# Kernel optimization log

Hardware: AMD Instinct MI355X
Metric: run time of the kernel (lower is better)

## Reference

```python
import jax, jax.numpy as jnp
import numpy as np

ROPE_BASE = 10000.0


def _rope_cos_sin(n, d, dtype):
    # standard llama-style rotary embedding over head dim d
    inv_freq = 1.0 / (ROPE_BASE ** (jnp.arange(0, d, 2, dtype=jnp.float32) / d))
    t = jnp.arange(n, dtype=jnp.float32)
    freqs = jnp.einsum('n,f->nf', t, inv_freq)          # [N, d/2]
    emb = jnp.concatenate([freqs, freqs], axis=-1)      # [N, d]
    return jnp.cos(emb).astype(dtype), jnp.sin(emb).astype(dtype)


def _rotate_half(x):
    x1, x2 = jnp.split(x, 2, axis=-1)
    return jnp.concatenate([-x2, x1], axis=-1)


def _apply_rope(x, cos, sin):
    # x: [B, H, N, D]; cos/sin: [N, D] broadcast over B, H
    return x * cos + _rotate_half(x) * sin


def setup_inputs() -> dict:
    key = jax.random.key(0)
    k1, k2, k3 = jax.random.split(key, 3)
    B, N, dim = 2, 2048, 1024
    heads, dim_head = 16, 64
    inner = heads * dim_head
    x = jax.random.normal(k1, (B, N, dim), dtype=jnp.float32)
    w_qkv = jax.random.normal(k2, (dim, 3 * inner), dtype=jnp.float32) * (dim ** -0.5)
    w_out = jax.random.normal(k3, (inner, dim), dtype=jnp.float32) * (inner ** -0.5)
    return {"x": x, "w_qkv": w_qkv, "w_out": w_out}


def reference(x, w_qkv, w_out):
    B, N, _ = x.shape
    heads, dim_head = 16, 64
    qkv = jnp.einsum('bnd,de->bne', x, w_qkv)
    q, k, v = jnp.split(qkv, 3, axis=-1)
    def to_heads(t):
        return t.reshape(B, N, heads, dim_head).transpose(0, 2, 1, 3)  # [B,H,N,D]
    q, k, v = to_heads(q), to_heads(k), to_heads(v)
    cos, sin = _rope_cos_sin(N, dim_head, x.dtype)
    q = _apply_rope(q, cos, sin)
    k = _apply_rope(k, cos, sin)
    scale = dim_head ** -0.5
    scores = jnp.einsum('bhqd,bhkd->bhqk', q, k) * scale   # [B,H,N,N], non-causal
    attn = jax.nn.softmax(scores, axis=-1)
    out = jnp.einsum('bhqk,bhkd->bhqd', attn, v)
    out = out.transpose(0, 2, 1, 3).reshape(B, N, heads * dim_head)
    return jnp.einsum('bne,ed->bnd', out, w_out)
```

## Files before the change

### kernel.cpp

```cpp
#include <hip/hip_runtime.h>

typedef __attribute__((ext_vector_type(8))) short bf16x8;
typedef __attribute__((ext_vector_type(4))) float f32x4;

#define MFMA(a, b, c) __builtin_amdgcn_mfma_f32_16x16x32_bf16(a, b, c, 0, 0, 0)

__device__ __forceinline__ unsigned short f2bf(float f) {
    unsigned u = __builtin_bit_cast(unsigned, f);
    u += 0x7fffu + ((u >> 16) & 1u);
    return (unsigned short)(u >> 16);
}

__device__ __forceinline__ void gload16(const unsigned short* g, unsigned short* l) {
    __builtin_amdgcn_global_load_lds(
        (const __attribute__((address_space(1))) void*)g,
        (__attribute__((address_space(3))) void*)l, 16, 0, 0);
}

__device__ __forceinline__ unsigned pack_bf16(float lo, float hi) {
    unsigned a = __builtin_bit_cast(unsigned, lo) + 0x8000u;
    unsigned b = __builtin_bit_cast(unsigned, hi) + 0x8000u;
    return __builtin_amdgcn_perm(b, a, 0x07060302);
}


__global__ __launch_bounds__(256) void cvt_bf16(const float* __restrict__ in,
                                                unsigned short* __restrict__ out, int n) {
    int i = (blockIdx.x * 256 + threadIdx.x) * 4;
    if (i < n) {
        float4 f = *(const float4*)(in + i);
        ushort4 u;
        u.x = f2bf(f.x); u.y = f2bf(f.y); u.z = f2bf(f.z); u.w = f2bf(f.w);
        *(ushort4*)(out + i) = u;
    }
}

__global__ __launch_bounds__(256) void transpose_cvt(const float* __restrict__ in,
                                                     unsigned short* __restrict__ out,
                                                     int R, int C) {
    __shared__ float tile[32][33];
    const int c0 = blockIdx.x * 32, r0 = blockIdx.y * 32;
    const int tr = threadIdx.x >> 3;
    const int j4 = (threadIdx.x & 7) * 4;
    float4 f = *(const float4*)(in + (size_t)(r0 + tr) * C + c0 + j4);
    tile[tr][j4 + 0] = f.x; tile[tr][j4 + 1] = f.y;
    tile[tr][j4 + 2] = f.z; tile[tr][j4 + 3] = f.w;
    __syncthreads();
    ushort4 u;
    u.x = f2bf(tile[j4 + 0][tr]); u.y = f2bf(tile[j4 + 1][tr]);
    u.z = f2bf(tile[j4 + 2][tr]); u.w = f2bf(tile[j4 + 3][tr]);
    *(ushort4*)(out + (size_t)(c0 + tr) * R + r0 + j4) = u;
}

__global__ __launch_bounds__(256) void rope_tab(float* __restrict__ cosT,
                                                float* __restrict__ sinT) {
    int i = blockIdx.x * 256 + threadIdx.x;
    int n = i >> 5, f = i & 31;
    float ang = (float)n * exp2f((float)f * -0.4152410118609203f);
    float s, c;
    sincosf(ang, &s, &c);
    cosT[i] = c; sinT[i] = s;
}


template <int EPI>
__global__ __launch_bounds__(256, 3) void gemm_bt(const unsigned short* __restrict__ A,
                                                  const unsigned short* __restrict__ Bt,
                                                  int K, int Ncols,
                                                  unsigned short* __restrict__ oq,
                                                  unsigned short* __restrict__ ok,
                                                  unsigned short* __restrict__ ovt,
                                                  float* __restrict__ of,
                                                  const float* __restrict__ cosT,
                                                  const float* __restrict__ sinT) {
    __shared__ unsigned short As[2][128 * 32];
    __shared__ unsigned short Bs[2][128 * 32];
    const int tid = threadIdx.x;
    const int w = tid >> 6, lane = tid & 63, quad = lane >> 4, cc = lane & 15;
    const int wm = w >> 1, wn = w & 1;
    const int m0 = blockIdx.y * 128, n0 = blockIdx.x * 128;

    size_t aoff[2], boff[2];
#pragma unroll
    for (int t = 0; t < 2; t++) {
        int S = w * 128 + t * 64 + lane;
        int row = S >> 2;
        int c = (S & 3) ^ ((row >> 1) & 3);
        aoff[t] = (size_t)(m0 + row) * K + c * 8;
        boff[t] = (size_t)(n0 + row) * K + c * 8;
    }

#pragma unroll
    for (int t = 0; t < 2; t++) {
        gload16(A + aoff[t], &As[0][(w * 2 + t) * 512]);
        gload16(Bt + boff[t], &Bs[0][(w * 2 + t) * 512]);
    }
    __syncthreads();

    f32x4 acc[4][4] = {};
    const int rpos = (quad ^ ((cc >> 1) & 3)) * 8;
    const int nkt = K >> 5;

    for (int kt = 0; kt < nkt; kt++) {
        const int pb = kt & 1;
        if (kt < nkt - 1) {
            const int ko = (kt + 1) * 32;
#pragma unroll
            for (int t = 0; t < 2; t++) {
                gload16(A + aoff[t] + ko, &As[pb ^ 1][(w * 2 + t) * 512]);
                gload16(Bt + boff[t] + ko, &Bs[pb ^ 1][(w * 2 + t) * 512]);
            }
        }
        bf16x8 af[4], bf[4];
#pragma unroll
        for (int i = 0; i < 4; i++)
            af[i] = *(const bf16x8*)&As[pb][(wm * 64 + i * 16 + cc) * 32 + rpos];
#pragma unroll
        for (int i = 0; i < 4; i++)
            bf[i] = *(const bf16x8*)&Bs[pb][(wn * 64 + i * 16 + cc) * 32 + rpos];
#pragma unroll
        for (int i = 0; i < 4; i++)
#pragma unroll
            for (int j = 0; j < 4; j++)
                acc[i][j] = MFMA(af[i], bf[j], acc[i][j]);
        __syncthreads();
    }

    if (EPI == 0) {
        const int e0 = n0 + wn * 64;
        const int which = e0 >> 10;
        const int h = (e0 >> 6) & 15;
        if (which < 2) {
            unsigned short* dst = (which == 0) ? oq : ok;
            const float postscale = (which == 0) ? 0.125f : 1.0f;
#pragma unroll
            for (int mf = 0; mf < 4; mf++) {
#pragma unroll
                for (int r = 0; r < 4; r++) {
                    int mg = m0 + wm * 64 + mf * 16 + quad * 4 + r;
                    int nseq = mg & 2047, b = mg >> 11;
                    float vals[4];
#pragma unroll
                    for (int nf = 0; nf < 4; nf++) vals[nf] = acc[mf][nf][r];
                    size_t rowbase = ((size_t)(b * 16 + h) * 2048 + nseq) * 64;
#pragma unroll
                    for (int nf = 0; nf < 4; nf++) {
                        int d = nf * 16 + cc;
                        int f = d & 31;
                        float cs = cosT[nseq * 32 + f];
                        float sn = sinT[nseq * 32 + f];
                        float partner = vals[nf ^ 2];
                        float outv = (vals[nf] * cs +
                                      ((nf < 2) ? -partner : partner) * sn) * postscale;
                        dst[rowbase + d] = f2bf(outv);
                    }
                }
            }
        } else {
#pragma unroll
            for (int mf = 0; mf < 4; mf++) {
                int mg0 = m0 + wm * 64 + mf * 16 + quad * 4;
                int b = mg0 >> 11, nseq = mg0 & 2047;
#pragma unroll
                for (int nf = 0; nf < 4; nf++) {
                    int d = nf * 16 + cc;
                    ushort4 pk;
                    pk.x = f2bf(acc[mf][nf][0]);
                    pk.y = f2bf(acc[mf][nf][1]);
                    pk.z = f2bf(acc[mf][nf][2]);
                    pk.w = f2bf(acc[mf][nf][3]);
                    *(ushort4*)(ovt + ((size_t)(b * 16 + h) * 64 + d) * 2048 + nseq) = pk;
                }
            }
        }
    } else {
#pragma unroll
        for (int mf = 0; mf < 4; mf++)
#pragma unroll
            for (int nf = 0; nf < 4; nf++)
#pragma unroll
                for (int r = 0; r < 4; r++) {
                    int mg = m0 + wm * 64 + mf * 16 + quad * 4 + r;
                    of[(size_t)mg * Ncols + n0 + wn * 64 + nf * 16 + cc] = acc[mf][nf][r];
                }
    }
}


__global__ __launch_bounds__(256, 2) void attn(const unsigned short* __restrict__ q,
                                               const unsigned short* __restrict__ k,
                                               const unsigned short* __restrict__ vt,
                                               unsigned short* __restrict__ o) {
    __shared__ unsigned short ks[2][64 * 64];
    __shared__ unsigned short vs[2][64 * 64];
    __shared__ unsigned short ps[128 * 72];
    __shared__ float rsb[128];
    const int tid = threadIdx.x;
    const int w = tid >> 6, lane = tid & 63, quad = lane >> 4, cc = lane & 15;
    const int bh = blockIdx.x & 31, qt = blockIdx.x >> 5;

    const unsigned short* qg = q + ((size_t)bh * 2048 + qt * 128 + w * 32) * 64;
    bf16x8 aq[2][2];
#pragma unroll
    for (int mf = 0; mf < 2; mf++)
#pragma unroll
        for (int kc = 0; kc < 2; kc++)
            aq[mf][kc] = *(const bf16x8*)(qg + (mf * 16 + cc) * 64 + kc * 32 + quad * 8);

    int koff[2], voff[2];
#pragma unroll
    for (int t = 0; t < 2; t++) {
        int S = w * 128 + t * 64 + lane;
        int row = S >> 3;
        int c = (S & 7) ^ (row & 7);
        koff[t] = row * 64 + c * 8;
        voff[t] = row * 2048 + c * 8;
    }

    const unsigned short* kg0 = k + (size_t)bh * 2048 * 64;
    const unsigned short* vg0 = vt + (size_t)bh * 64 * 2048;

#pragma unroll
    for (int t = 0; t < 2; t++) {
        gload16(kg0 + koff[t], &ks[0][(w * 2 + t) * 512]);
        gload16(vg0 + voff[t], &vs[0][(w * 2 + t) * 512]);
    }
    __syncthreads();

    f32x4 oacc[2][4] = {};
    float rs[2] = {};

    for (int kt = 0; kt < 32; kt++) {
        const int pb = kt & 1;
        if (kt < 31) {
            const unsigned short* kb = kg0 + (kt + 1) * 4096;
            const unsigned short* vb = vg0 + (kt + 1) * 64;
#pragma unroll
            for (int t = 0; t < 2; t++) {
                gload16(kb + koff[t], &ks[pb ^ 1][(w * 2 + t) * 512]);
                gload16(vb + voff[t], &vs[pb ^ 1][(w * 2 + t) * 512]);
            }
        }

        f32x4 s2[2][4] = {};
#pragma unroll
        for (int kc = 0; kc < 2; kc++) {
#pragma unroll
            for (int nf = 0; nf < 4; nf++) {
                bf16x8 bk = *(const bf16x8*)&ks[pb][(nf * 16 + cc) * 64 +
                                                    ((kc * 4 + quad) ^ (cc & 7)) * 8];
                s2[0][nf] = MFMA(bk, aq[0][kc], s2[0][nf]);
                s2[1][nf] = MFMA(bk, aq[1][kc], s2[1][nf]);
            }
        }

#pragma unroll
        for (int mf = 0; mf < 2; mf++) {
#pragma unroll
            for (int nf = 0; nf < 4; nf++) {
                float p0 = __builtin_amdgcn_exp2f(
                    __builtin_fmaf(s2[mf][nf][0], 1.44269504f, -11.54156036f));
                float p1 = __builtin_amdgcn_exp2f(
                    __builtin_fmaf(s2[mf][nf][1], 1.44269504f, -11.54156036f));
                float p2 = __builtin_amdgcn_exp2f(
                    __builtin_fmaf(s2[mf][nf][2], 1.44269504f, -11.54156036f));
                float p3 = __builtin_amdgcn_exp2f(
                    __builtin_fmaf(s2[mf][nf][3], 1.44269504f, -11.54156036f));
                rs[mf] += (p0 + p1) + (p2 + p3);
                uint2 pk;
                pk.x = pack_bf16(p0, p1);
                pk.y = pack_bf16(p2, p3);
                *(uint2*)&ps[(w * 32 + mf * 16 + cc) * 72 + nf * 16 + quad * 4] = pk;
            }
        }

#pragma unroll
        for (int kc = 0; kc < 2; kc++) {
            bf16x8 ap[2];
            ap[0] = *(const bf16x8*)&ps[(w * 32 + cc) * 72 + kc * 32 + quad * 8];
            ap[1] = *(const bf16x8*)&ps[(w * 32 + 16 + cc) * 72 + kc * 32 + quad * 8];
#pragma unroll
            for (int df = 0; df < 4; df++) {
                bf16x8 bv = *(const bf16x8*)&vs[pb][(df * 16 + cc) * 64 +
                                                    ((kc * 4 + quad) ^ (cc & 7)) * 8];
                oacc[0][df] = MFMA(ap[0], bv, oacc[0][df]);
                oacc[1][df] = MFMA(ap[1], bv, oacc[1][df]);
            }
        }

        __syncthreads();
    }

#pragma unroll
    for (int mf = 0; mf < 2; mf++) {
        rs[mf] += __shfl_xor(rs[mf], 16, 64);
        rs[mf] += __shfl_xor(rs[mf], 32, 64);
    }
    if (quad == 0) {
        rsb[w * 32 + cc] = rs[0];
        rsb[w * 32 + 16 + cc] = rs[1];
    }

#pragma unroll
    for (int mf = 0; mf < 2; mf++) {
        f32x4 rv = *(const f32x4*)&rsb[w * 32 + mf * 16 + quad * 4];
        f32x4 inv;
#pragma unroll
        for (int r = 0; r < 4; r++) inv[r] = 1.0f / rv[r];
#pragma unroll
        for (int r = 0; r < 4; r++)
#pragma unroll
            for (int df = 0; df < 4; df++)
                ps[(w * 32 + mf * 16 + quad * 4 + r) * 72 + df * 16 + cc] =
                    f2bf(oacc[mf][df][r] * inv[r]);
    }
    __syncthreads();
    {
        const int b = bh >> 4, h = bh & 15;
        int row = tid >> 1, hf = tid & 1;
        unsigned short* og =
            o + ((size_t)(b * 2048 + qt * 128 + row)) * 1024 + h * 64 + hf * 32;
#pragma unroll
        for (int j = 0; j < 4; j++)
            *(uint4*)(og + j * 8) = *(const uint4*)&ps[row * 72 + hf * 32 + j * 8];
    }
}


extern "C" void kernel_launch(void* const* d_in, const int* in_sizes, int n_in,
                              void* d_out, int out_size, void* d_ws, size_t ws_size,
                              hipStream_t stream) {
    const float* x = (const float*)d_in[0];
    const float* w_qkv = (const float*)d_in[1];
    const float* w_out = (const float*)d_in[2];
    float* out = (float*)d_out;

    unsigned short* xb    = (unsigned short*)d_ws;
    unsigned short* wqkvT = xb + 4096 * 1024;
    unsigned short* woutT = wqkvT + 3072 * 1024;
    unsigned short* qb    = woutT + 1024 * 1024;
    unsigned short* kb    = qb + 2 * 16 * 2048 * 64;
    unsigned short* vtb   = kb + 2 * 16 * 2048 * 64;
    unsigned short* ob    = vtb + 2 * 16 * 2048 * 64;
    float* cosT = (float*)(ob + 4096 * 1024);
    float* sinT = cosT + 2048 * 32;

    rope_tab<<<256, 256, 0, stream>>>(cosT, sinT);
    cvt_bf16<<<4096, 256, 0, stream>>>(x, xb, 4096 * 1024);
    transpose_cvt<<<dim3(96, 32), 256, 0, stream>>>(w_qkv, wqkvT, 1024, 3072);
    transpose_cvt<<<dim3(32, 32), 256, 0, stream>>>(w_out, woutT, 1024, 1024);
    gemm_bt<0><<<dim3(24, 32), 256, 0, stream>>>(xb, wqkvT, 1024, 3072,
                                                 qb, kb, vtb, nullptr, cosT, sinT);
    attn<<<512, 256, 0, stream>>>(qb, kb, vtb, ob);
    gemm_bt<1><<<dim3(8, 32), 256, 0, stream>>>(ob, woutT, 1024, 1024,
                                                nullptr, nullptr, nullptr, out,
                                                nullptr, nullptr);
}
```

Baseline: 190.3 us.

## Keep softmax probabilities in registers and feed PV via 16x16x16 MFMA

The exp'd score tile, laid out as the MFMA output, is now packed into bf16x4 registers and used directly as an operand of the 16x16x16 bf16 MFMA. This removes the LDS round-trip for P and its shared buffer, and computes the transposed O tile so row sums stay in lane registers. The epilogue writes O straight to global without staging through LDS or a block barrier. It also drops the P buffer's LDS footprint and raises launch bounds to 4 blocks/CU. The trade-off is twice as many smaller MFMAs, narrower V loads, and uncoalesced 8-byte output stores.

```diff
diff --git a/kernel.cpp b/kernel.cpp
--- a/kernel.cpp
+++ b/kernel.cpp
@@ -1,9 +1,11 @@
 #include <hip/hip_runtime.h>
 
 typedef __attribute__((ext_vector_type(8))) short bf16x8;
+typedef __attribute__((ext_vector_type(4))) short bf16x4;
 typedef __attribute__((ext_vector_type(4))) float f32x4;
 
 #define MFMA(a, b, c) __builtin_amdgcn_mfma_f32_16x16x32_bf16(a, b, c, 0, 0, 0)
+#define MFMA16(a, b, c) __builtin_amdgcn_mfma_f32_16x16x16bf16_1k(a, b, c, 0, 0, 0)
 
 __device__ __forceinline__ unsigned short f2bf(float f) {
     unsigned u = __builtin_bit_cast(unsigned, f);
@@ -187,14 +189,12 @@
 }
 
 
-__global__ __launch_bounds__(256, 2) void attn(const unsigned short* __restrict__ q,
+__global__ __launch_bounds__(256, 4) void attn(const unsigned short* __restrict__ q,
                                                const unsigned short* __restrict__ k,
                                                const unsigned short* __restrict__ vt,
                                                unsigned short* __restrict__ o) {
     __shared__ unsigned short ks[2][64 * 64];
     __shared__ unsigned short vs[2][64 * 64];
-    __shared__ unsigned short ps[128 * 72];
-    __shared__ float rsb[128];
     const int tid = threadIdx.x;
     const int w = tid >> 6, lane = tid & 63, quad = lane >> 4, cc = lane & 15;
     const int bh = blockIdx.x & 31, qt = blockIdx.x >> 5;
@@ -254,6 +254,7 @@
             }
         }
 
+        bf16x4 pkr[2][4];
 #pragma unroll
         for (int mf = 0; mf < 2; mf++) {
 #pragma unroll
@@ -267,24 +268,22 @@
                 float p3 = __builtin_amdgcn_exp2f(
                     __builtin_fmaf(s2[mf][nf][3], 1.44269504f, -11.54156036f));
                 rs[mf] += (p0 + p1) + (p2 + p3);
-                uint2 pk;
-                pk.x = pack_bf16(p0, p1);
-                pk.y = pack_bf16(p2, p3);
-                *(uint2*)&ps[(w * 32 + mf * 16 + cc) * 72 + nf * 16 + quad * 4] = pk;
-            }
-        }
-
-#pragma unroll
-        for (int kc = 0; kc < 2; kc++) {
-            bf16x8 ap[2];
-            ap[0] = *(const bf16x8*)&ps[(w * 32 + cc) * 72 + kc * 32 + quad * 8];
-            ap[1] = *(const bf16x8*)&ps[(w * 32 + 16 + cc) * 72 + kc * 32 + quad * 8];
+                uint2 u;
+                u.x = pack_bf16(p0, p1);
+                u.y = pack_bf16(p2, p3);
+                pkr[mf][nf] = __builtin_bit_cast(bf16x4, u);
+            }
+        }
+
+#pragma unroll
+        for (int nf = 0; nf < 4; nf++) {
 #pragma unroll
             for (int df = 0; df < 4; df++) {
-                bf16x8 bv = *(const bf16x8*)&vs[pb][(df * 16 + cc) * 64 +
-                                                    ((kc * 4 + quad) ^ (cc & 7)) * 8];
-                oacc[0][df] = MFMA(ap[0], bv, oacc[0][df]);
-                oacc[1][df] = MFMA(ap[1], bv, oacc[1][df]);
+                bf16x4 bv = *(const bf16x4*)&vs[pb][(df * 16 + cc) * 64 +
+                                                    (((nf * 2 + (quad >> 1)) ^ (cc & 7)) * 8) +
+                                                    (quad & 1) * 4];
+                oacc[0][df] = MFMA16(bv, pkr[0][nf], oacc[0][df]);
+                oacc[1][df] = MFMA16(bv, pkr[1][nf], oacc[1][df]);
             }
         }
 
@@ -296,33 +295,21 @@
         rs[mf] += __shfl_xor(rs[mf], 16, 64);
         rs[mf] += __shfl_xor(rs[mf], 32, 64);
     }
-    if (quad == 0) {
-        rsb[w * 32 + cc] = rs[0];
-        rsb[w * 32 + 16 + cc] = rs[1];
-    }
-
-#pragma unroll
-    for (int mf = 0; mf < 2; mf++) {
-        f32x4 rv = *(const f32x4*)&rsb[w * 32 + mf * 16 + quad * 4];
-        f32x4 inv;
-#pragma unroll
-        for (int r = 0; r < 4; r++) inv[r] = 1.0f / rv[r];
-#pragma unroll
-        for (int r = 0; r < 4; r++)
-#pragma unroll
-            for (int df = 0; df < 4; df++)
-                ps[(w * 32 + mf * 16 + quad * 4 + r) * 72 + df * 16 + cc] =
-                    f2bf(oacc[mf][df][r] * inv[r]);
-    }
-    __syncthreads();
+
     {
         const int b = bh >> 4, h = bh & 15;
-        int row = tid >> 1, hf = tid & 1;
-        unsigned short* og =
-            o + ((size_t)(b * 2048 + qt * 128 + row)) * 1024 + h * 64 + hf * 32;
-#pragma unroll
-        for (int j = 0; j < 4; j++)
-            *(uint4*)(og + j * 8) = *(const uint4*)&ps[row * 72 + hf * 32 + j * 8];
+        unsigned short* og = o + ((size_t)(b * 2048 + qt * 128 + w * 32)) * 1024 + h * 64;
+#pragma unroll
+        for (int mf = 0; mf < 2; mf++) {
+            float inv = 1.0f / rs[mf];
+#pragma unroll
+            for (int df = 0; df < 4; df++) {
+                uint2 u;
+                u.x = pack_bf16(oacc[mf][df][0] * inv, oacc[mf][df][1] * inv);
+                u.y = pack_bf16(oacc[mf][df][2] * inv, oacc[mf][df][3] * inv);
+                *(uint2*)(og + (size_t)(mf * 16 + cc) * 1024 + df * 16 + quad * 4) = u;
+            }
+        }
     }
 }
 
```

Measured after the change: 198.4 us. 1.04x slower.
